# Kernel tuning notes

Measured on AMD Instinct MI355X. Metric: run time of the kernel, lower is better.

## Reference

```python
import jax, jax.numpy as jnp
import numpy as np

LEVELS = ((64, 176), (32, 88), (16, 44), (8, 22))
S_TOTAL = sum(h * w for h, w in LEVELS)  # 14960
C = 128; HH = 8; HD = 16; R = 4; L = 4; P = 8
G = 32; PC_MIN = -4.0; PC_MAX = 4.0
NUM_CLASSES = 17; PROP = 3 + 3 + 4 + 1 + NUM_CLASSES  # 28


def _ln(x, g, b):
    m = x.mean(-1, keepdims=True)
    v = ((x - m) ** 2).mean(-1, keepdims=True)
    return (x - m) * jax.lax.rsqrt(v + 1e-5) * g + b


def setup_inputs() -> dict:
    key = jax.random.key(0)
    ks = jax.random.split(key, 20)
    B, N, CAM = 1, 1024, 6
    d = {}
    d['query'] = jax.random.normal(ks[0], (B, N, C), jnp.float32)
    d['gaussian_props'] = jax.random.normal(ks[1], (B, N, PROP), jnp.float32)
    d['ms_feats'] = jax.random.normal(ks[2], (B, CAM, S_TOTAL, C), jnp.float32)
    d['depth_maps'] = jax.random.uniform(ks[3], (B, CAM, 64, 176), jnp.float32, 0.5, 50.0)
    d['lidar2img'] = jax.random.normal(ks[4], (B, CAM, 4, 4), jnp.float32)
    d['img_h'] = 256
    d['img_w'] = 704
    w = lambda k, shp: jax.random.normal(k, shp, jnp.float32) * 0.02
    d['W_sc'] = w(ks[5], (3, 3, 3, C, C)); d['b_sc'] = jnp.zeros((C,), jnp.float32)
    d['sc_g'] = jnp.ones((C,), jnp.float32); d['sc_b'] = jnp.zeros((C,), jnp.float32)
    d['ref_off_w'] = w(ks[6], (C, R * 3)); d['ref_off_b'] = jnp.zeros((R * 3,), jnp.float32)
    d['off_w'] = w(ks[7], (C, HH * R * L * P * 2)); d['off_b'] = jnp.zeros((HH * R * L * P * 2,), jnp.float32)
    d['aw_w'] = w(ks[8], (C, HH * R * L * P)); d['aw_b'] = jnp.zeros((HH * R * L * P,), jnp.float32)
    d['val_w'] = w(ks[9], (C, C)); d['val_b'] = jnp.zeros((C,), jnp.float32)
    d['out_w'] = w(ks[10], (C, C)); d['out_b'] = jnp.zeros((C,), jnp.float32)
    d['an_g'] = jnp.ones((C,), jnp.float32); d['an_b'] = jnp.zeros((C,), jnp.float32)
    d['f1_w'] = w(ks[11], (C, 4 * C)); d['f1_b'] = jnp.zeros((4 * C,), jnp.float32)
    d['f2_w'] = w(ks[12], (4 * C, C)); d['f2_b'] = jnp.zeros((C,), jnp.float32)
    d['fn_g'] = jnp.ones((C,), jnp.float32); d['fn_b'] = jnp.zeros((C,), jnp.float32)
    d['p1_w'] = w(ks[13], (C, C)); d['p1_b'] = jnp.zeros((C,), jnp.float32)
    d['p2_w'] = w(ks[14], (C, PROP)); d['p2_b'] = jnp.zeros((PROP,), jnp.float32)
    return d


def _forward(query, gaussian_props, ms_feats, depth_maps, lidar2img,
             W_sc, b_sc, sc_g, sc_b, ref_off_w, ref_off_b, off_w, off_b,
             aw_w, aw_b, val_w, val_b, out_w, out_b, an_g, an_b,
             f1_w, f1_b, f2_w, f2_b, fn_g, fn_b, p1_w, p1_b, p2_w, p2_b,
             img_h, img_w):
    B, N, _ = query.shape
    CAM = ms_feats.shape[1]
    means = gaussian_props[..., :3]
    # ---- SparseConv3DBlock: scatter-mean voxelization, 3x3x3 conv, gather back ----
    vs = (PC_MAX - PC_MIN) / G
    vox = jnp.clip(jnp.floor((means - PC_MIN) / vs).astype(jnp.int32), 0, G - 1)
    flat = (vox[..., 0] * G + vox[..., 1]) * G + vox[..., 2]  # [B,N]
    bi = jnp.arange(B)[:, None]
    grid = jnp.zeros((B, G * G * G, C), query.dtype).at[bi, flat].add(query)
    cnt = jnp.zeros((B, G * G * G, 1), query.dtype).at[bi, flat].add(1.0)
    grid = (grid / jnp.maximum(cnt, 1.0)).reshape(B, G, G, G, C)
    grid = jax.lax.conv_general_dilated(grid, W_sc, (1, 1, 1), 'SAME',
                                        dimension_numbers=('NDHWC', 'DHWIO', 'NDHWC')) + b_sc
    grid = jax.nn.gelu(grid).reshape(B, G * G * G, C)
    query = _ln(query + grid[bi, flat], sc_g, sc_b)
    # ---- DeformableAttention3D ----
    fW = jnp.asarray(img_w, query.dtype); fH = jnp.asarray(img_h, query.dtype)
    ref3d = means[:, :, None, :] + (query @ ref_off_w + ref_off_b).reshape(B, N, R, 3)
    pts = jnp.concatenate([ref3d, jnp.ones_like(ref3d[..., :1])], -1)
    proj = jnp.einsum('bcij,bnrj->bcnri', lidar2img, pts)  # [B,CAM,N,R,4]
    z = proj[..., 2]; zc = jnp.maximum(z, 1e-5)
    u = proj[..., 0] / zc; v = proj[..., 1] / zc
    valid = (z > 1e-5) & (u >= 0) & (u < fW) & (v >= 0) & (v < fH)
    Hd, Wd = depth_maps.shape[2], depth_maps.shape[3]
    iu = jnp.clip((u / fW * Wd).astype(jnp.int32), 0, Wd - 1)
    iv = jnp.clip((v / fH * Hd).astype(jnp.int32), 0, Hd - 1)
    ds = jnp.take_along_axis(depth_maps.reshape(B, CAM, Hd * Wd),
                             (iv * Wd + iu).reshape(B, CAM, N * R), axis=2).reshape(B, CAM, N, R)
    wmask = jnp.exp(-jnp.abs(z - ds)) * valid.astype(query.dtype)  # [B,CAM,N,R]
    ref2 = jnp.stack([u / fW, v / fH], -1)  # [B,CAM,N,R,2]
    offs = (query @ off_w + off_b).reshape(B, N, HH, R, L, P, 2)
    attn = jax.nn.softmax((query @ aw_w + aw_b).reshape(B, N, HH, R * L * P), -1)
    attn = attn.reshape(B, N, HH, R, L, P)
    value = (ms_feats @ val_w + val_b).reshape(B, CAM, S_TOTAL, HH, HD)
    out = jnp.zeros((B, N, HH, HD), query.dtype)
    s0 = 0
    for l, (Hl, Wl) in enumerate(LEVELS):
        sz = Hl * Wl
        vl = value[:, :, s0:s0 + sz].transpose(0, 1, 3, 2, 4).reshape(B * CAM, HH, sz, HD)
        s0 += sz
        off_l = offs[:, :, :, :, l]  # [B,N,HH,R,P,2]
        loc = ref2[:, :, :, None, :, None, :] + off_l[:, None] / jnp.array([Wl, Hl], query.dtype)
        # loc: [B,CAM,N,HH,R,P,2] in normalized coords
        x = (loc[..., 0] * Wl - 0.5).transpose(0, 1, 3, 2, 4, 5).reshape(B * CAM, HH, N * R * P)
        y = (loc[..., 1] * Hl - 0.5).transpose(0, 1, 3, 2, 4, 5).reshape(B * CAM, HH, N * R * P)
        x0 = jnp.floor(x); y0 = jnp.floor(y); wx = x - x0; wy = y - y0
        x0i = jnp.clip(x0.astype(jnp.int32), 0, Wl - 1)
        x1i = jnp.clip(x0.astype(jnp.int32) + 1, 0, Wl - 1)
        y0i = jnp.clip(y0.astype(jnp.int32), 0, Hl - 1)
        y1i = jnp.clip(y0.astype(jnp.int32) + 1, 0, Hl - 1)
        g = lambda ix, iy: jnp.take_along_axis(vl, (iy * Wl + ix)[..., None], axis=2)
        samp = (((1 - wx) * (1 - wy))[..., None] * g(x0i, y0i)
                + (wx * (1 - wy))[..., None] * g(x1i, y0i)
                + ((1 - wx) * wy)[..., None] * g(x0i, y1i)
                + (wx * wy)[..., None] * g(x1i, y1i))  # [B*CAM,HH,N*R*P,HD]
        samp = samp.reshape(B, CAM, HH, N, R, P, HD)
        ws = attn[:, :, :, :, l, :][:, None].transpose(0, 1, 3, 2, 4, 5) * wmask[:, :, None, :, :, None]
        out = out + jnp.einsum('bchnrp,bchnrpd->bnhd', ws, samp)
    attn_out = out.reshape(B, N, C) @ out_w + out_b
    query = _ln(query + attn_out, an_g, an_b)
    query = _ln(query + (jax.nn.gelu(query @ f1_w + f1_b) @ f2_w + f2_b), fn_g, fn_b)
    props = gaussian_props + (jax.nn.gelu(query @ p1_w + p1_b) @ p2_w + p2_b)
    return query, props


def reference(query, gaussian_props, ms_feats, depth_maps, lidar2img,
              W_sc, b_sc, sc_g, sc_b, ref_off_w, ref_off_b, off_w, off_b,
              aw_w, aw_b, val_w, val_b, out_w, out_b, an_g, an_b,
              f1_w, f1_b, f2_w, f2_b, fn_g, fn_b, p1_w, p1_b, p2_w, p2_b,
              img_h, img_w):
    return _forward(query, gaussian_props, ms_feats, depth_maps, lidar2img,
                    W_sc, b_sc, sc_g, sc_b, ref_off_w, ref_off_b, off_w, off_b,
                    aw_w, aw_b, val_w, val_b, out_w, out_b, an_g, an_b,
                    f1_w, f1_b, f2_w, f2_b, fn_g, fn_b, p1_w, p1_b, p2_w, p2_b,
                    img_h, img_w)
```

## Files before the change

kernel.cpp:

```cpp
#include <hip/hip_runtime.h>
#include <hip/hip_bf16.h>
#include <math.h>

#define NQ    1024
#define CC    128
#define CAM   6
#define RR    4
#define LL    4
#define PP    8
#define HHD   8
#define HDD   16
#define GG    32
#define S_TOT 14960
#define PROPN 28
#define NTAP  27

typedef __attribute__((ext_vector_type(8))) short bf16x8;
typedef __attribute__((ext_vector_type(4))) float f32x4;

__device__ __forceinline__ float gelu_tanh(float x) {
    return 0.5f * x * (1.0f + tanhf(0.7978845608028654f * (x + 0.044715f * x * x * x)));
}

__device__ __forceinline__ unsigned short f2bf(float f) {
    union { float f; unsigned int u; } x; x.f = f;
    unsigned int r = (x.u + 0x7FFFu + ((x.u >> 16) & 1u)) >> 16;
    return (unsigned short)r;
}

__device__ __forceinline__ float bf2f(short s) {
    union { unsigned int u; float f; } x;
    x.u = ((unsigned int)(unsigned short)s) << 16;
    return x.f;
}

__global__ void k_wt_scatter(const float* __restrict__ Wsc, unsigned short* __restrict__ WscT,
                             const float* __restrict__ valw, unsigned short* __restrict__ valwT,
                             const float* __restrict__ outw, unsigned short* __restrict__ outwT,
                             const float* __restrict__ p1w, unsigned short* __restrict__ p1wT,
                             const float* __restrict__ f1w, unsigned short* __restrict__ f1wT,
                             const float* __restrict__ f2w, unsigned short* __restrict__ f2wT,
                             const float* __restrict__ offw, unsigned short* __restrict__ offwT,
                             const float* __restrict__ aww, unsigned short* __restrict__ awwT,
                             const float* __restrict__ p2w, unsigned short* __restrict__ p2wT,
                             const float* __restrict__ p2b, float* __restrict__ p2bp,
                             const float* __restrict__ qin, const float* __restrict__ gp,
                             float* __restrict__ grid, float* __restrict__ cnt,
                             int* __restrict__ flatidx) {
    __shared__ float t[64][65];
    __shared__ int sflat[2];
    int z = blockIdx.z;
    int tid = threadIdx.x;

    if (z >= 63) {
        int half = tid >> 7, c = tid & 127;
        int n = ((z - 63) * 4 + (blockIdx.x * 2 + blockIdx.y)) * 2 + half;
        if (c == 0) {
            float mx = gp[n * PROPN + 0], my = gp[n * PROPN + 1], mz = gp[n * PROPN + 2];
            int vx = (int)floorf((mx + 4.0f) * 4.0f);
            int vy = (int)floorf((my + 4.0f) * 4.0f);
            int vz = (int)floorf((mz + 4.0f) * 4.0f);
            vx = min(max(vx, 0), GG - 1);
            vy = min(max(vy, 0), GG - 1);
            vz = min(max(vz, 0), GG - 1);
            int f = (vx * GG + vy) * GG + vz;
            sflat[half] = f;
            flatidx[n] = f;
            atomicAdd(&cnt[f], 1.0f);
        }
        __syncthreads();
        atomicAdd(&grid[(size_t)sflat[half] * CC + c], qin[(size_t)n * CC + c]);
        return;
    }

    int n0 = blockIdx.x * 64, k0 = blockIdx.y * 64;
    if (z == 62) {
#pragma unroll
        for (int it = 0; it < 16; ++it) {
            int idx = tid + it * 256;
            int r = idx >> 6, c = idx & 63;
            t[r][c] = (n0 + c < PROPN) ? p2w[(size_t)(k0 + r) * PROPN + n0 + c] : 0.f;
        }
        __syncthreads();
#pragma unroll
        for (int it = 0; it < 16; ++it) {
            int idx = tid + it * 256;
            int r = idx >> 6, c = idx & 63;
            p2wT[(size_t)(n0 + r) * 128 + k0 + c] = f2bf(t[c][r]);
        }
        if (blockIdx.x == 0 && blockIdx.y == 0 && tid < 128)
            p2bp[tid] = (tid < PROPN) ? p2b[tid] : 0.f;
        return;
    }
    const float* src; unsigned short* dst; int ss, ds;
    if (z < 27)       { src = Wsc + (size_t)z * 16384; dst = WscT + (size_t)z * 16384; ss = 128; ds = 128; }
    else if (z == 27) { src = valw; dst = valwT; ss = 128; ds = 128; }
    else if (z == 28) { src = outw; dst = outwT; ss = 128; ds = 128; }
    else if (z == 29) { src = p1w;  dst = p1wT;  ss = 128; ds = 128; }
    else if (z < 34)  { int q = z - 30; src = f1w + q * 128; dst = f1wT + (size_t)q * 16384; ss = 512;  ds = 128; }
    else if (z < 38)  { int q = z - 34; src = f2w + (size_t)q * 16384; dst = f2wT + q * 128; ss = 128;  ds = 512; }
    else if (z < 54)  { int q = z - 38; src = offw + q * 128; dst = offwT + (size_t)q * 16384; ss = 2048; ds = 128; }
    else              { int q = z - 54; src = aww + q * 128;  dst = awwT + (size_t)q * 16384; ss = 1024; ds = 128; }
#pragma unroll
    for (int it = 0; it < 16; ++it) {
        int idx = tid + it * 256;
        int r = idx >> 6, c = idx & 63;
        t[r][c] = src[(size_t)(k0 + r) * ss + n0 + c];
    }
    __syncthreads();
#pragma unroll
    for (int it = 0; it < 16; ++it) {
        int idx = tid + it * 256;
        int r = idx >> 6, c = idx & 63;
        dst[(size_t)(n0 + r) * ds + k0 + c] = f2bf(t[c][r]);
    }
}

__global__ __launch_bounds__(256) void k_conv1m(
    const float* __restrict__ grid, const float* __restrict__ cnt,
    const int* __restrict__ flatidx, const unsigned short* __restrict__ WT,
    float* __restrict__ convacc27) {
    __shared__ bf16x8 As[128 * 16];
    __shared__ bf16x8 Bs[128 * 16];
    __shared__ int   nbase[128];
    __shared__ float nscale[128];
    int tid = threadIdx.x;
    int tap = blockIdx.y;
    int q0 = blockIdx.x * 128;
    int dz = tap / 9 - 1, dy = (tap / 3) % 3 - 1, dx = tap % 3 - 1;

    if (tid < 128) {
        int f = flatidx[q0 + tid];
        int nx = (f >> 10) + dz, ny = ((f >> 5) & 31) + dy, nz = (f & 31) + dx;
        bool ok = (nx >= 0 && nx < GG && ny >= 0 && ny < GG && nz >= 0 && nz < GG);
        int nf = ok ? (nx * GG + ny) * GG + nz : 0;
        nbase[tid] = nf;
        nscale[tid] = ok ? 1.0f / fmaxf(cnt[nf], 1.0f) : 0.f;
    }
    __syncthreads();
#pragma unroll
    for (int it = 0; it < 8; ++it) {
        int idx = tid + it * 256;
        int m = idx >> 4, c = idx & 15;
        const float* p = grid + (size_t)nbase[m] * CC + c * 8;
        float s = nscale[m];
        float4 a = *(const float4*)p;
        float4 b = *(const float4*)(p + 4);
        bf16x8 u;
        u[0] = (short)f2bf(a.x * s); u[1] = (short)f2bf(a.y * s);
        u[2] = (short)f2bf(a.z * s); u[3] = (short)f2bf(a.w * s);
        u[4] = (short)f2bf(b.x * s); u[5] = (short)f2bf(b.y * s);
        u[6] = (short)f2bf(b.z * s); u[7] = (short)f2bf(b.w * s);
        As[m * 16 + (c ^ (m & 15))] = u;
    }
    const unsigned short* Wt = WT + (size_t)tap * CC * CC;
#pragma unroll
    for (int it = 0; it < 8; ++it) {
        int idx = tid + it * 256;
        int n = idx >> 4, c = idx & 15;
        bf16x8 w = *(const bf16x8*)(Wt + (size_t)n * CC + c * 8);
        Bs[n * 16 + (c ^ (n & 15))] = w;
    }
    __syncthreads();

    int lane = tid & 63, wv = tid >> 6;
    int wr = (wv >> 1) * 64, wc = (wv & 1) * 64;
    int r = lane & 15, q = lane >> 4;
    f32x4 acc[4][4];
#pragma unroll
    for (int i = 0; i < 4; ++i)
#pragma unroll
        for (int j = 0; j < 4; ++j)
#pragma unroll
            for (int e = 0; e < 4; ++e) acc[i][j][e] = 0.f;
#pragma unroll
    for (int ks = 0; ks < 4; ++ks) {
        bf16x8 bfr[4];
#pragma unroll
        for (int j = 0; j < 4; ++j)
            bfr[j] = Bs[(wc + j * 16 + r) * 16 + ((ks * 4 + q) ^ r)];
#pragma unroll
        for (int i = 0; i < 4; ++i) {
            bf16x8 af = As[(wr + i * 16 + r) * 16 + ((ks * 4 + q) ^ r)];
#pragma unroll
            for (int j = 0; j < 4; ++j)
                acc[i][j] = __builtin_amdgcn_mfma_f32_16x16x32_bf16(af, bfr[j], acc[i][j], 0, 0, 0);
        }
    }
    float* dst = convacc27 + (size_t)tap * NQ * CC;
#pragma unroll
    for (int i = 0; i < 4; ++i)
#pragma unroll
        for (int e = 0; e < 4; ++e) {
            int m = q0 + wr + i * 16 + q * 4 + e;
#pragma unroll
            for (int j = 0; j < 4; ++j) {
                int col = wc + j * 16 + r;
                dst[(size_t)m * CC + col] = acc[i][j][e];
            }
        }
}

__global__ void k_ln_conv_proj(const float* __restrict__ a, const float* __restrict__ convacc27,
                               const float* __restrict__ bconv,
                               const float* __restrict__ g, const float* __restrict__ be,
                               float* __restrict__ out,
                               const float* __restrict__ refw, const float* __restrict__ refb,
                               const float* __restrict__ gp, const float* __restrict__ l2i,
                               const float* __restrict__ depth,
                               const int* __restrict__ ih, const int* __restrict__ iw,
                               float* __restrict__ wm, float* __restrict__ r2u,
                               float* __restrict__ r2v) {
    int n = blockIdx.x, c = threadIdx.x;
    float apart = 0.f;
#pragma unroll
    for (int t = 0; t < NTAP; ++t) apart += convacc27[((size_t)t * NQ + n) * CC + c];
    float x = a[n * CC + c] + gelu_tanh(apart + bconv[c]);
    __shared__ float red[CC];
    __shared__ float qrow[CC];
    __shared__ float ro[12];
    red[c] = x;
    __syncthreads();
    for (int s = 64; s >= 1; s >>= 1) { if (c < s) red[c] += red[c + s]; __syncthreads(); }
    float m = red[0] * (1.0f / CC);
    __syncthreads();
    float d = x - m;
    red[c] = d * d;
    __syncthreads();
    for (int s = 64; s >= 1; s >>= 1) { if (c < s) red[c] += red[c + s]; __syncthreads(); }
    float v = red[0] * (1.0f / CC);
    float qv = d * rsqrtf(v + 1e-5f) * g[c] + be[c];
    out[n * CC + c] = qv;
    qrow[c] = qv;
    __syncthreads();
    if (c < 12) {
        float s = refb[c];
#pragma unroll 4
        for (int k = 0; k < 128; ++k) s += qrow[k] * refw[k * 12 + c];
        ro[c] = s;
    }
    __syncthreads();
    if (c < 24) {
        int cam = c >> 2, r = c & 3;
        float fH = (float)(*ih), fW = (float)(*iw);
        const float* M = l2i + cam * 16;
        float px = gp[n * PROPN + 0] + ro[r * 3 + 0];
        float py = gp[n * PROPN + 1] + ro[r * 3 + 1];
        float pz = gp[n * PROPN + 2] + ro[r * 3 + 2];
        float p0 = M[0] * px + M[1] * py + M[2]  * pz + M[3];
        float p1 = M[4] * px + M[5] * py + M[6]  * pz + M[7];
        float p2 = M[8] * px + M[9] * py + M[10] * pz + M[11];
        float zc = fmaxf(p2, 1e-5f);
        float u = p0 / zc, vv = p1 / zc;
        bool valid = (p2 > 1e-5f) && (u >= 0.f) && (u < fW) && (vv >= 0.f) && (vv < fH);
        int iu = min(max((int)(u / fW * 176.f), 0), 175);
        int iv = min(max((int)(vv / fH * 64.f), 0), 63);
        float ds = depth[cam * 64 * 176 + iv * 176 + iu];
        int o = cam * (NQ * RR) + n * RR + r;
        wm[o]  = valid ? expf(-fabsf(p2 - ds)) : 0.f;
        r2u[o] = u / fW;
        r2v[o] = vv / fH;
    }
}

__global__ __launch_bounds__(256) void k_qhead(
    const float* __restrict__ A,
    const unsigned short* __restrict__ offwT, const float* __restrict__ offb,
    unsigned short* __restrict__ offsb,
    const unsigned short* __restrict__ awwT, const float* __restrict__ awb,
    unsigned short* __restrict__ attn)
{
    __shared__ bf16x8 As[128 * 16];
    __shared__ bf16x8 Bs[128 * 16];
    __shared__ float xrow[128 * 128];
    bool isoff = blockIdx.x < 16;
    int n0 = (isoff ? blockIdx.x : (blockIdx.x - 16)) * 128;
    const unsigned short* WT = isoff ? offwT : awwT;
    int m0 = blockIdx.y * 128;
    int tid = threadIdx.x, lane = tid & 63, wv = tid >> 6;
    int wr = (wv >> 1) * 64, wc = (wv & 1) * 64;
    int r = lane & 15, q = lane >> 4;

#pragma unroll
    for (int it = 0; it < 8; ++it) {
        int idx = tid + it * 256;
        int m = idx >> 4, c = idx & 15;
        const float* p = A + (size_t)(m0 + m) * 128 + c * 8;
        float4 a = *(const float4*)p;
        float4 b = *(const float4*)(p + 4);
        bf16x8 u;
        u[0] = (short)f2bf(a.x); u[1] = (short)f2bf(a.y);
        u[2] = (short)f2bf(a.z); u[3] = (short)f2bf(a.w);
        u[4] = (short)f2bf(b.x); u[5] = (short)f2bf(b.y);
        u[6] = (short)f2bf(b.z); u[7] = (short)f2bf(b.w);
        As[m * 16 + (c ^ (m & 15))] = u;
    }
#pragma unroll
    for (int it = 0; it < 8; ++it) {
        int idx = tid + it * 256;
        int n = idx >> 4, c = idx & 15;
        Bs[n * 16 + (c ^ (n & 15))] = *(const bf16x8*)(WT + (size_t)(n0 + n) * 128 + c * 8);
    }
    __syncthreads();

    f32x4 acc[4][4];
#pragma unroll
    for (int i = 0; i < 4; ++i)
#pragma unroll
        for (int j = 0; j < 4; ++j)
#pragma unroll
            for (int e = 0; e < 4; ++e) acc[i][j][e] = 0.f;
#pragma unroll
    for (int ks = 0; ks < 4; ++ks) {
        bf16x8 bfr[4];
#pragma unroll
        for (int j = 0; j < 4; ++j)
            bfr[j] = Bs[(wc + j * 16 + r) * 16 + ((ks * 4 + q) ^ r)];
#pragma unroll
        for (int i = 0; i < 4; ++i) {
            bf16x8 af = As[(wr + i * 16 + r) * 16 + ((ks * 4 + q) ^ r)];
#pragma unroll
            for (int j = 0; j < 4; ++j)
                acc[i][j] = __builtin_amdgcn_mfma_f32_16x16x32_bf16(af, bfr[j], acc[i][j], 0, 0, 0);
        }
    }

    if (isoff) {
#pragma unroll
        for (int i = 0; i < 4; ++i)
#pragma unroll
            for (int e = 0; e < 4; ++e) {
                int m = m0 + wr + i * 16 + q * 4 + e;
#pragma unroll
                for (int j = 0; j < 4; ++j) {
                    int col = n0 + wc + j * 16 + r;
                    offsb[(size_t)m * 2048 + col] = f2bf(acc[i][j][e] + offb[col]);
                }
            }
    } else {
#pragma unroll
        for (int i = 0; i < 4; ++i)
#pragma unroll
            for (int e = 0; e < 4; ++e) {
                int ml = wr + i * 16 + q * 4 + e;
#pragma unroll
                for (int j = 0; j < 4; ++j) {
                    int cl = wc + j * 16 + r;
                    xrow[ml * 128 + cl] = acc[i][j][e] + awb[n0 + cl];
                }
            }
        __syncthreads();
        int row = tid >> 1, s = tid & 1;
        float* xr = xrow + row * 128;
        float mx = -1e30f;
#pragma unroll
        for (int e = s; e < 128; e += 2) mx = fmaxf(mx, xr[e]);
        mx = fmaxf(mx, __shfl_xor(mx, 1, 2));
        float sum = 0.f;
#pragma unroll
        for (int e = s; e < 128; e += 2) { float ee = expf(xr[e] - mx); xr[e] = ee; sum += ee; }
        sum += __shfl_xor(sum, 1, 2);
        float inv = 1.0f / sum;
        unsigned short* orow = attn + (size_t)(m0 + row) * 1024 + n0;
#pragma unroll
        for (int e = s; e < 128; e += 2) orow[e] = f2bf(xr[e] * inv);
    }
}

__global__ __launch_bounds__(256) void k_valproj(
    const float* __restrict__ A, const unsigned short* __restrict__ WT,
    const float* __restrict__ bias, unsigned short* __restrict__ out, int M)
{
    __shared__ bf16x8 Bs[128 * 16];
    __shared__ unsigned short Os[64 * 128];
    __shared__ float sbias[128];
    int tid = threadIdx.x;
    int m0 = blockIdx.x * 64;
    int lane = tid & 63, wv = tid >> 6;
    int r = lane & 15, q = lane >> 4;

#pragma unroll
    for (int it = 0; it < 8; ++it) {
        int idx = tid + it * 256;
        int n = idx >> 4, c = idx & 15;
        Bs[n * 16 + (c ^ (n & 15))] = *(const bf16x8*)(WT + (size_t)n * 128 + c * 8);
    }
    if (tid < 128) sbias[tid] = bias[tid];
    __syncthreads();

    int row = m0 + wv * 16 + r;
    int mg = min(row, M - 1);
    const float* pA = A + (size_t)mg * 128;

    f32x4 acc[8];
#pragma unroll
    for (int j = 0; j < 8; ++j)
#pragma unroll
        for (int e = 0; e < 4; ++e) acc[j][e] = 0.f;

#pragma unroll
    for (int ks = 0; ks < 4; ++ks) {
        const float* p = pA + ks * 32 + q * 8;
        float4 a = *(const float4*)p;
        float4 b = *(const float4*)(p + 4);
        bf16x8 af;
        af[0] = (short)f2bf(a.x); af[1] = (short)f2bf(a.y);
        af[2] = (short)f2bf(a.z); af[3] = (short)f2bf(a.w);
        af[4] = (short)f2bf(b.x); af[5] = (short)f2bf(b.y);
        af[6] = (short)f2bf(b.z); af[7] = (short)f2bf(b.w);
        bf16x8 bfr[8];
#pragma unroll
        for (int j = 0; j < 8; ++j)
            bfr[j] = Bs[(j * 16 + r) * 16 + ((ks * 4 + q) ^ r)];
#pragma unroll
        for (int j = 0; j < 8; ++j)
            acc[j] = __builtin_amdgcn_mfma_f32_16x16x32_bf16(af, bfr[j], acc[j], 0, 0, 0);
    }

#pragma unroll
    for (int j = 0; j < 8; ++j)
#pragma unroll
        for (int e = 0; e < 4; ++e) {
            int rl = wv * 16 + q * 4 + e;
            Os[rl * 128 + j * 16 + r] = f2bf(acc[j][e] + sbias[j * 16 + r]);
        }
    __syncthreads();
#pragma unroll
    for (int it = 0; it < 2; ++it) {
        int idx = tid + it * 256;
        int rl = idx & 63, h = idx >> 6;
        int m = m0 + rl;
        if (m < M) {
            int cam = m / S_TOT;
            int s = m - cam * S_TOT;
            int pos, HW, sb;
            if (s < 11264)      { pos = s;          HW = 11264; sb = 0; }
            else if (s < 14080) { pos = s - 11264;  HW = 2816;  sb = 11264; }
            else if (s < 14784) { pos = s - 14080;  HW = 704;   sb = 14080; }
            else                { pos = s - 14784;  HW = 176;   sb = 14784; }
            size_t dst = ((size_t)cam * S_TOT + sb) * CC
                       + (size_t)h * (HW * HDD) + (size_t)pos * HDD;
            *(bf16x8*)(out + dst)     = *(const bf16x8*)&Os[rl * 128 + h * 16];
            *(bf16x8*)(out + dst + 8) = *(const bf16x8*)&Os[rl * 128 + h * 16 + 8];
        }
    }
}

__global__ void k_sample(const unsigned short* __restrict__ value,
                         const unsigned short* __restrict__ offsb,
                         const unsigned short* __restrict__ attn,
                         const float* __restrict__ wm,
                         const float* __restrict__ r2u, const float* __restrict__ r2v,
                         float* __restrict__ sampout) {
    const int Wl_[4] = {176, 88, 44, 22};
    const int Hl_[4] = {64, 32, 16, 8};
    const int s0_[4] = {0, 11264, 14080, 14784};
    int n = blockIdx.x, tid = threadIdx.x;
    __shared__ float s_attn[1024];
    __shared__ float s_offs[2048];
    __shared__ float s_wm[24], s_ru[24], s_rv[24];

    if (tid < 128) {
        bf16x8 v = *(const bf16x8*)(attn + (size_t)n * 1024 + tid * 8);
#pragma unroll
        for (int d = 0; d < 8; ++d) s_attn[tid * 8 + d] = bf2f(v[d]);
    }
    {
        bf16x8 v = *(const bf16x8*)(offsb + (size_t)n * 2048 + tid * 8);
#pragma unroll
        for (int d = 0; d < 8; ++d) s_offs[tid * 8 + d] = bf2f(v[d]);
    }
    if (tid < 24) {
        int cam = tid >> 2, r = tid & 3;
        int o = cam * (NQ * RR) + n * RR + r;
        s_wm[tid] = wm[o]; s_ru[tid] = r2u[o]; s_rv[tid] = r2v[o];
    }
    __syncthreads();

    int h = tid >> 5, slot = tid & 31;
    int l = slot >> 3, p = slot & 7;
    int Wl = Wl_[l], Hl = Hl_[l];
    float fWl = (float)Wl, fHl = (float)Hl;
    size_t planeC = (size_t)s0_[l] * CC + (size_t)h * (Hl * Wl * HDD);
    float acc[16];
#pragma unroll
    for (int d = 0; d < 16; ++d) acc[d] = 0.f;

    for (int cr = 0; cr < 24; ++cr) {
        int cam = cr >> 2, r = cr & 3;
        float ws = s_attn[h * 128 + r * 32 + l * 8 + p] * s_wm[cr];
        if (ws == 0.f) continue;
        float ox = s_offs[h * 256 + r * 64 + l * 16 + p * 2 + 0];
        float oy = s_offs[h * 256 + r * 64 + l * 16 + p * 2 + 1];
        float x = s_ru[cr] * fWl + ox - 0.5f;
        float y = s_rv[cr] * fHl + oy - 0.5f;
        float xf = floorf(x), yf = floorf(y);
        float wx = x - xf, wy = y - yf;
        int x0 = min(max((int)xf, 0), Wl - 1);
        int x1 = min(max((int)xf + 1, 0), Wl - 1);
        int y0 = min(max((int)yf, 0), Hl - 1);
        int y1 = min(max((int)yf + 1, 0), Hl - 1);
        const unsigned short* base = value + (size_t)cam * S_TOT * CC + planeC;
        const unsigned short* p00 = base + (size_t)(y0 * Wl + x0) * HDD;
        const unsigned short* p01 = base + (size_t)(y0 * Wl + x1) * HDD;
        const unsigned short* p10 = base + (size_t)(y1 * Wl + x0) * HDD;
        const unsigned short* p11 = base + (size_t)(y1 * Wl + x1) * HDD;
        float w00 = ws * (1.f - wx) * (1.f - wy);
        float w01 = ws * wx * (1.f - wy);
        float w10 = ws * (1.f - wx) * wy;
        float w11 = ws * wx * wy;
        bf16x8 va0 = *(const bf16x8*)p00, va1 = *(const bf16x8*)(p00 + 8);
        bf16x8 vb0 = *(const bf16x8*)p01, vb1 = *(const bf16x8*)(p01 + 8);
        bf16x8 vc0 = *(const bf16x8*)p10, vc1 = *(const bf16x8*)(p10 + 8);
        bf16x8 vd0 = *(const bf16x8*)p11, vd1 = *(const bf16x8*)(p11 + 8);
#pragma unroll
        for (int d = 0; d < 8; ++d)
            acc[d] += w00 * bf2f(va0[d]) + w01 * bf2f(vb0[d]) + w10 * bf2f(vc0[d]) + w11 * bf2f(vd0[d]);
#pragma unroll
        for (int d = 0; d < 8; ++d)
            acc[8 + d] += w00 * bf2f(va1[d]) + w01 * bf2f(vb1[d]) + w10 * bf2f(vc1[d]) + w11 * bf2f(vd1[d]);
    }

#pragma unroll
    for (int d = 0; d < 16; ++d) {
        float a = acc[d];
#pragma unroll
        for (int s = 16; s >= 1; s >>= 1) a += __shfl_xor(a, s, 32);
        acc[d] = a;
    }
    if (slot == 0) {
#pragma unroll
        for (int d = 0; d < 16; ++d)
            sampout[(size_t)n * CC + h * HDD + d] = acc[d];
    }
}

__global__ __launch_bounds__(256) void k_tail(
    const float* __restrict__ sampout,
    const unsigned short* __restrict__ outwT, const float* __restrict__ outb,
    const float* __restrict__ q1, const float* __restrict__ ang, const float* __restrict__ anb,
    const unsigned short* __restrict__ f1wT, const float* __restrict__ f1b,
    const unsigned short* __restrict__ f2wT, const float* __restrict__ f2b,
    const float* __restrict__ fng, const float* __restrict__ fnb,
    const unsigned short* __restrict__ p1wT, const float* __restrict__ p1b,
    const unsigned short* __restrict__ p2wT, const float* __restrict__ p2bp,
    const float* __restrict__ gp, float* __restrict__ outq, float* __restrict__ outp)
{
    __shared__ bf16x8 As[16 * 16];
    __shared__ bf16x8 Aff[16 * 64];
    __shared__ float xrow[16 * 128];
    __shared__ float q2s[16 * 128];
    unsigned short* Affu = (unsigned short*)Aff;
    unsigned short* As2u = (unsigned short*)Aff;
    int tid = threadIdx.x, m0 = blockIdx.x * 16;
    int lane = tid & 63, wv = tid >> 6;
    int wc = wv * 32;
    int r = lane & 15, q = lane >> 4;
    int lrow = tid >> 4, ls = tid & 15;

    bf16x8 b1[2][4];
#pragma unroll
    for (int j = 0; j < 2; ++j)
#pragma unroll
        for (int ks = 0; ks < 4; ++ks)
            b1[j][ks] = *(const bf16x8*)(outwT + (size_t)(wc + j * 16 + r) * 128 + (ks * 4 + q) * 8);

    {
        int m = tid >> 4, c = tid & 15;
        const float* p = sampout + (size_t)(m0 + m) * 128 + c * 8;
        float4 a = *(const float4*)p;
        float4 b = *(const float4*)(p + 4);
        bf16x8 u;
        u[0] = (short)f2bf(a.x); u[1] = (short)f2bf(a.y);
        u[2] = (short)f2bf(a.z); u[3] = (short)f2bf(a.w);
        u[4] = (short)f2bf(b.x); u[5] = (short)f2bf(b.y);
        u[6] = (short)f2bf(b.z); u[7] = (short)f2bf(b.w);
        As[m * 16 + (c ^ m)] = u;
    }
    __syncthreads();

    f32x4 acc[2];
    bf16x8 a4[4];
#pragma unroll
    for (int ks = 0; ks < 4; ++ks) a4[ks] = As[r * 16 + ((ks * 4 + q) ^ r)];
#pragma unroll
    for (int j = 0; j < 2; ++j)
#pragma unroll
        for (int e = 0; e < 4; ++e) acc[j][e] = 0.f;
#pragma unroll
    for (int ks = 0; ks < 4; ++ks)
#pragma unroll
        for (int j = 0; j < 2; ++j)
            acc[j] = __builtin_amdgcn_mfma_f32_16x16x32_bf16(a4[ks], b1[j][ks], acc[j], 0, 0, 0);
#pragma unroll
    for (int e = 0; e < 4; ++e) {
        int ml = q * 4 + e;
#pragma unroll
        for (int j = 0; j < 2; ++j) {
            int cl = wc + j * 16 + r;
            xrow[ml * 128 + cl] = acc[j][e] + outb[cl] + q1[(size_t)(m0 + ml) * 128 + cl];
        }
    }
    __syncthreads();

    {
        float* xr = xrow + lrow * 128;
        float sum = 0.f;
#pragma unroll
        for (int e = ls; e < 128; e += 16) sum += xr[e];
#pragma unroll
        for (int d = 8; d; d >>= 1) sum += __shfl_xor(sum, d, 16);
        float mean = sum * (1.0f / 128.0f);
        float var = 0.f;
#pragma unroll
        for (int e = ls; e < 128; e += 16) { float dd = xr[e] - mean; var += dd * dd; }
#pragma unroll
        for (int d = 8; d; d >>= 1) var += __shfl_xor(var, d, 16);
        float rstd = rsqrtf(var * (1.0f / 128.0f) + 1e-5f);
#pragma unroll
        for (int e = ls; e < 128; e += 16)
            q2s[lrow * 128 + e] = (xr[e] - mean) * rstd * ang[e] + anb[e];
    }
    __syncthreads();
    {
        int m = tid >> 4, c = tid & 15;
        const float* p = q2s + m * 128 + c * 8;
        bf16x8 u;
#pragma unroll
        for (int d = 0; d < 8; ++d) u[d] = (short)f2bf(p[d]);
        As[m * 16 + (c ^ m)] = u;
    }
    __syncthreads();

#pragma unroll
    for (int ks = 0; ks < 4; ++ks) a4[ks] = As[r * 16 + ((ks * 4 + q) ^ r)];
    bf16x8 bcur[2][4];
#pragma unroll
    for (int j = 0; j < 2; ++j)
#pragma unroll
        for (int ks = 0; ks < 4; ++ks)
            bcur[j][ks] = *(const bf16x8*)(f1wT + (size_t)(wc + j * 16 + r) * 128 + (ks * 4 + q) * 8);
#pragma unroll
    for (int nt = 0; nt < 4; ++nt) {
        bf16x8 bnx[2][4];
        if (nt < 3) {
#pragma unroll
            for (int j = 0; j < 2; ++j)
#pragma unroll
                for (int ks = 0; ks < 4; ++ks)
                    bnx[j][ks] = *(const bf16x8*)(f1wT + (size_t)(nt + 1) * 16384
                                                  + (size_t)(wc + j * 16 + r) * 128 + (ks * 4 + q) * 8);
        }
#pragma unroll
        for (int j = 0; j < 2; ++j)
#pragma unroll
            for (int e = 0; e < 4; ++e) acc[j][e] = 0.f;
#pragma unroll
        for (int ks = 0; ks < 4; ++ks)
#pragma unroll
            for (int j = 0; j < 2; ++j)
                acc[j] = __builtin_amdgcn_mfma_f32_16x16x32_bf16(a4[ks], bcur[j][ks], acc[j], 0, 0, 0);
#pragma unroll
        for (int e = 0; e < 4; ++e) {
            int ml = q * 4 + e;
#pragma unroll
            for (int j = 0; j < 2; ++j) {
                int col = nt * 128 + wc + j * 16 + r;
                float v = gelu_tanh(acc[j][e] + f1b[col]);
                Affu[(ml * 64 + ((col >> 3) ^ ml)) * 8 + (col & 7)] = f2bf(v);
            }
        }
        if (nt < 3) {
#pragma unroll
            for (int j = 0; j < 2; ++j)
#pragma unroll
                for (int ks = 0; ks < 4; ++ks) bcur[j][ks] = bnx[j][ks];
        }
    }
    __syncthreads();

#pragma unroll
    for (int j = 0; j < 2; ++j)
#pragma unroll
        for (int e = 0; e < 4; ++e) acc[j][e] = 0.f;
#pragma unroll
    for (int j = 0; j < 2; ++j)
#pragma unroll
        for (int ks = 0; ks < 4; ++ks)
            bcur[j][ks] = *(const bf16x8*)(f2wT + (size_t)(wc + j * 16 + r) * 512 + (ks * 4 + q) * 8);
#pragma unroll
    for (int kc = 0; kc < 4; ++kc) {
        bf16x8 bnx[2][4];
        if (kc < 3) {
#pragma unroll
            for (int j = 0; j < 2; ++j)
#pragma unroll
                for (int ks = 0; ks < 4; ++ks)
                    bnx[j][ks] = *(const bf16x8*)(f2wT + (size_t)(wc + j * 16 + r) * 512
                                                  + ((kc + 1) * 16 + ks * 4 + q) * 8);
        }
#pragma unroll
        for (int ks = 0; ks < 4; ++ks) {
            bf16x8 af = Aff[r * 64 + ((kc * 16 + ks * 4 + q) ^ r)];
#pragma unroll
            for (int j = 0; j < 2; ++j)
                acc[j] = __builtin_amdgcn_mfma_f32_16x16x32_bf16(af, bcur[j][ks], acc[j], 0, 0, 0);
        }
        if (kc < 3) {
#pragma unroll
            for (int j = 0; j < 2; ++j)
#pragma unroll
                for (int ks = 0; ks < 4; ++ks) bcur[j][ks] = bnx[j][ks];
        }
    }
#pragma unroll
    for (int e = 0; e < 4; ++e) {
        int ml = q * 4 + e;
#pragma unroll
        for (int j = 0; j < 2; ++j) {
            int cl = wc + j * 16 + r;
            xrow[ml * 128 + cl] = acc[j][e] + f2b[cl] + q2s[ml * 128 + cl];
        }
    }
    __syncthreads();

    {
        float* xr = xrow + lrow * 128;
        float sum = 0.f;
#pragma unroll
        for (int e = ls; e < 128; e += 16) sum += xr[e];
#pragma unroll
        for (int d = 8; d; d >>= 1) sum += __shfl_xor(sum, d, 16);
        float mean = sum * (1.0f / 128.0f);
        float var = 0.f;
#pragma unroll
        for (int e = ls; e < 128; e += 16) { float dd = xr[e] - mean; var += dd * dd; }
#pragma unroll
        for (int d = 8; d; d >>= 1) var += __shfl_xor(var, d, 16);
        float rstd = rsqrtf(var * (1.0f / 128.0f) + 1e-5f);
        float* oq = outq + (size_t)(m0 + lrow) * 128;
#pragma unroll
        for (int e = ls; e < 128; e += 16) {
            float v = (xr[e] - mean) * rstd * fng[e] + fnb[e];
            oq[e] = v;
            q2s[lrow * 128 + e] = v;
        }
    }
    __syncthreads();
    {
        int m = tid >> 4, c = tid & 15;
        const float* p = q2s + m * 128 + c * 8;
        bf16x8 u;
#pragma unroll
        for (int d = 0; d < 8; ++d) u[d] = (short)f2bf(p[d]);
        As[m * 16 + (c ^ m)] = u;
    }
    __syncthreads();

#pragma unroll
    for (int ks = 0; ks < 4; ++ks) a4[ks] = As[r * 16 + ((ks * 4 + q) ^ r)];
#pragma unroll
    for (int j = 0; j < 2; ++j) {
#pragma unroll
        for (int ks = 0; ks < 4; ++ks)
            bcur[j][ks] = *(const bf16x8*)(p1wT + (size_t)(wc + j * 16 + r) * 128 + (ks * 4 + q) * 8);
#pragma unroll
        for (int e = 0; e < 4; ++e) acc[j][e] = 0.f;
    }
#pragma unroll
    for (int j = 0; j < 2; ++j)
#pragma unroll
        for (int ks = 0; ks < 4; ++ks)
            b1[j][ks] = *(const bf16x8*)(p2wT + (size_t)(wc + j * 16 + r) * 128 + (ks * 4 + q) * 8);
#pragma unroll
    for (int ks = 0; ks < 4; ++ks)
#pragma unroll
        for (int j = 0; j < 2; ++j)
            acc[j] = __builtin_amdgcn_mfma_f32_16x16x32_bf16(a4[ks], bcur[j][ks], acc[j], 0, 0, 0);
#pragma unroll
    for (int e = 0; e < 4; ++e) {
        int ml = q * 4 + e;
#pragma unroll
        for (int j = 0; j < 2; ++j) {
            int cl = wc + j * 16 + r;
            float v = gelu_tanh(acc[j][e] + p1b[cl]);
            As2u[(ml * 16 + ((cl >> 3) ^ ml)) * 8 + (cl & 7)] = f2bf(v);
        }
    }
    __syncthreads();

#pragma unroll
    for (int j = 0; j < 2; ++j)
#pragma unroll
        for (int e = 0; e < 4; ++e) acc[j][e] = 0.f;
#pragma unroll
    for (int ks = 0; ks < 4; ++ks) {
        bf16x8 af = Aff[r * 16 + ((ks * 4 + q) ^ r)];
#pragma unroll
        for (int j = 0; j < 2; ++j)
            acc[j] = __builtin_amdgcn_mfma_f32_16x16x32_bf16(af, b1[j][ks], acc[j], 0, 0, 0);
    }
#pragma unroll
    for (int e = 0; e < 4; ++e) {
        int m = m0 + q * 4 + e;
#pragma unroll
        for (int j = 0; j < 2; ++j) {
            int cl = wc + j * 16 + r;
            if (cl < PROPN)
                outp[(size_t)m * PROPN + cl] = acc[j][e] + p2bp[cl] + gp[(size_t)m * PROPN + cl];
        }
    }
}

extern "C" void kernel_launch(void* const* d_in, const int* in_sizes, int n_in,
                              void* d_out, int out_size, void* d_ws, size_t ws_size,
                              hipStream_t stream) {
    const float* query = (const float*)d_in[0];
    const float* gp    = (const float*)d_in[1];
    const float* ms    = (const float*)d_in[2];
    const float* depth = (const float*)d_in[3];
    const float* l2i   = (const float*)d_in[4];
    const int*   ih    = (const int*)d_in[5];
    const int*   iw    = (const int*)d_in[6];
    const float* Wsc   = (const float*)d_in[7];
    const float* bsc   = (const float*)d_in[8];
    const float* scg   = (const float*)d_in[9];
    const float* scb   = (const float*)d_in[10];
    const float* refw  = (const float*)d_in[11];
    const float* refb  = (const float*)d_in[12];
    const float* offw  = (const float*)d_in[13];
    const float* offbi = (const float*)d_in[14];
    const float* aww   = (const float*)d_in[15];
    const float* awb   = (const float*)d_in[16];
    const float* valw  = (const float*)d_in[17];
    const float* valb  = (const float*)d_in[18];
    const float* outw  = (const float*)d_in[19];
    const float* outb  = (const float*)d_in[20];
    const float* ang   = (const float*)d_in[21];
    const float* anb   = (const float*)d_in[22];
    const float* f1w   = (const float*)d_in[23];
    const float* f1b   = (const float*)d_in[24];
    const float* f2w   = (const float*)d_in[25];
    const float* f2b   = (const float*)d_in[26];
    const float* fng   = (const float*)d_in[27];
    const float* fnb   = (const float*)d_in[28];
    const float* p1w   = (const float*)d_in[29];
    const float* p1b   = (const float*)d_in[30];
    const float* p2w   = (const float*)d_in[31];
    const float* p2b   = (const float*)d_in[32];

    float* outq = (float*)d_out;
    float* outp = outq + NQ * CC;

    float* ws = (float*)d_ws;
    size_t o = 0;
    float* grid    = ws + o; o += (size_t)GG * GG * GG * CC;
    float* cnt     = ws + o; o += GG * GG * GG;
    size_t zero_floats = o;
    int*   flatidx = (int*)(ws + o); o += NQ;
    float* convacc27 = ws + o; o += (size_t)NTAP * NQ * CC;
    float* q1      = ws + o; o += NQ * CC;
    float* wm      = ws + o; o += CAM * NQ * RR;
    float* r2u     = ws + o; o += CAM * NQ * RR;
    float* r2v     = ws + o; o += CAM * NQ * RR;
    float* sampout = ws + o; o += NQ * CC;
    float* p2bp    = ws + o; o += 128;
    unsigned short* u16base = (unsigned short*)(ws + o);
    size_t uo = 0;
    unsigned short* value = u16base + uo; uo += (size_t)CAM * S_TOT * CC;
    unsigned short* offsb = u16base + uo; uo += (size_t)NQ * 2048;
    unsigned short* attn  = u16base + uo; uo += (size_t)NQ * 1024;
    unsigned short* offwT = u16base + uo; uo += (size_t)2048 * 128;
    unsigned short* awwT  = u16base + uo; uo += (size_t)1024 * 128;
    unsigned short* valwT = u16base + uo; uo += 128 * 128;
    unsigned short* outwT = u16base + uo; uo += 128 * 128;
    unsigned short* f1wT  = u16base + uo; uo += 512 * 128;
    unsigned short* f2wT  = u16base + uo; uo += 128 * 512;
    unsigned short* p1wT  = u16base + uo; uo += 128 * 128;
    unsigned short* p2wT  = u16base + uo; uo += 128 * 128;
    unsigned short* WscT  = u16base + uo; uo += (size_t)27 * 128 * 128;
    (void)ws_size; (void)in_sizes; (void)n_in; (void)out_size;

    hipMemsetAsync(ws, 0, zero_floats * sizeof(float), stream);

    k_wt_scatter<<<dim3(2, 2, 63 + 128), 256, 0, stream>>>(
        Wsc, WscT, valw, valwT, outw, outwT, p1w, p1wT, f1w, f1wT, f2w, f2wT,
        offw, offwT, aww, awwT, p2w, p2wT, p2b, p2bp,
        query, gp, grid, cnt, flatidx);

    k_conv1m<<<dim3(8, 27), 256, 0, stream>>>(grid, cnt, flatidx, WscT, convacc27);
    k_ln_conv_proj<<<NQ, CC, 0, stream>>>(query, convacc27, bsc, scg, scb, q1,
                                          refw, refb, gp, l2i, depth, ih, iw, wm, r2u, r2v);

    k_qhead<<<dim3(24, 8), 256, 0, stream>>>(q1, offwT, offbi, offsb, awwT, awb, attn);
    k_valproj<<<(CAM * S_TOT + 63) / 64, 256, 0, stream>>>(ms, valwT, valb, value, CAM * S_TOT);
    k_sample<<<NQ, 256, 0, stream>>>(value, offsb, attn, wm, r2u, r2v, sampout);

    k_tail<<<64, 256, 0, stream>>>(sampout, outwT, outb, q1, ang, anb,
                                   f1wT, f1b, f2wT, f2b, fng, fnb,
                                   p1wT, p1b, p2wT, p2bp, gp, outq, outp);
}
```

Before: 243.6 us.

## Use row-major value layout, register softmax in qhead, and shuffle-based layernorm

The value projection now writes rows in natural [pos][channel] order instead of a head-planar layout, and the sampler addresses with stride CC. That turns the projection epilogue into contiguous writes, but each bilinear tap in the sampler becomes a 32-byte read spread across 256-byte rows. k_qhead drops the shared A tile and the 64KB xrow buffer: each wave converts A fragments straight from global memory and does the softmax in registers with cross-lane shuffles, which lowers LDS use and may allow higher occupancy. The layernorm in k_ln_conv_proj replaces its tree reductions through shared memory with wavefront shuffle reductions, using fewer barriers.

```diff
diff --git a/kernel.cpp b/kernel.cpp
--- a/kernel.cpp
+++ b/kernel.cpp
@@ -216,28 +216,31 @@
 #pragma unroll
     for (int t = 0; t < NTAP; ++t) apart += convacc27[((size_t)t * NQ + n) * CC + c];
     float x = a[n * CC + c] + gelu_tanh(apart + bconv[c]);
-    __shared__ float red[CC];
+    __shared__ float w4[4];
     __shared__ float qrow[CC];
     __shared__ float ro[12];
-    red[c] = x;
-    __syncthreads();
-    for (int s = 64; s >= 1; s >>= 1) { if (c < s) red[c] += red[c + s]; __syncthreads(); }
-    float m = red[0] * (1.0f / CC);
-    __syncthreads();
-    float d = x - m;
-    red[c] = d * d;
-    __syncthreads();
-    for (int s = 64; s >= 1; s >>= 1) { if (c < s) red[c] += red[c + s]; __syncthreads(); }
-    float v = red[0] * (1.0f / CC);
-    float qv = d * rsqrtf(v + 1e-5f) * g[c] + be[c];
+    float s = x;
+#pragma unroll
+    for (int d = 1; d < 64; d <<= 1) s += __shfl_xor(s, d);
+    if ((c & 63) == 0) w4[c >> 6] = s;
+    __syncthreads();
+    float m = (w4[0] + w4[1]) * (1.0f / CC);
+    float dd = x - m;
+    float v = dd * dd;
+#pragma unroll
+    for (int d = 1; d < 64; d <<= 1) v += __shfl_xor(v, d);
+    if ((c & 63) == 0) w4[2 + (c >> 6)] = v;
+    __syncthreads();
+    float var = (w4[2] + w4[3]) * (1.0f / CC);
+    float qv = dd * rsqrtf(var + 1e-5f) * g[c] + be[c];
     out[n * CC + c] = qv;
     qrow[c] = qv;
     __syncthreads();
     if (c < 12) {
-        float s = refb[c];
+        float sacc = refb[c];
 #pragma unroll 4
-        for (int k = 0; k < 128; ++k) s += qrow[k] * refw[k * 12 + c];
-        ro[c] = s;
+        for (int k = 0; k < 128; ++k) sacc += qrow[k] * refw[k * 12 + c];
+        ro[c] = sacc;
     }
     __syncthreads();
     if (c < 24) {
@@ -270,31 +273,15 @@
     const unsigned short* __restrict__ awwT, const float* __restrict__ awb,
     unsigned short* __restrict__ attn)
 {
-    __shared__ bf16x8 As[128 * 16];
     __shared__ bf16x8 Bs[128 * 16];
-    __shared__ float xrow[128 * 128];
     bool isoff = blockIdx.x < 16;
     int n0 = (isoff ? blockIdx.x : (blockIdx.x - 16)) * 128;
     const unsigned short* WT = isoff ? offwT : awwT;
     int m0 = blockIdx.y * 128;
     int tid = threadIdx.x, lane = tid & 63, wv = tid >> 6;
-    int wr = (wv >> 1) * 64, wc = (wv & 1) * 64;
     int r = lane & 15, q = lane >> 4;
-
-#pragma unroll
-    for (int it = 0; it < 8; ++it) {
-        int idx = tid + it * 256;
-        int m = idx >> 4, c = idx & 15;
-        const float* p = A + (size_t)(m0 + m) * 128 + c * 8;
-        float4 a = *(const float4*)p;
-        float4 b = *(const float4*)(p + 4);
-        bf16x8 u;
-        u[0] = (short)f2bf(a.x); u[1] = (short)f2bf(a.y);
-        u[2] = (short)f2bf(a.z); u[3] = (short)f2bf(a.w);
-        u[4] = (short)f2bf(b.x); u[5] = (short)f2bf(b.y);
-        u[6] = (short)f2bf(b.z); u[7] = (short)f2bf(b.w);
-        As[m * 16 + (c ^ (m & 15))] = u;
-    }
+    int mw = m0 + wv * 32;
+
 #pragma unroll
     for (int it = 0; it < 8; ++it) {
         int idx = tid + it * 256;
@@ -303,67 +290,77 @@
     }
     __syncthreads();
 
-    f32x4 acc[4][4];
-#pragma unroll
-    for (int i = 0; i < 4; ++i)
-#pragma unroll
-        for (int j = 0; j < 4; ++j)
+    f32x4 acc[2][8];
+#pragma unroll
+    for (int i = 0; i < 2; ++i)
+#pragma unroll
+        for (int j = 0; j < 8; ++j)
 #pragma unroll
             for (int e = 0; e < 4; ++e) acc[i][j][e] = 0.f;
+
 #pragma unroll
     for (int ks = 0; ks < 4; ++ks) {
-        bf16x8 bfr[4];
-#pragma unroll
-        for (int j = 0; j < 4; ++j)
-            bfr[j] = Bs[(wc + j * 16 + r) * 16 + ((ks * 4 + q) ^ r)];
-#pragma unroll
-        for (int i = 0; i < 4; ++i) {
-            bf16x8 af = As[(wr + i * 16 + r) * 16 + ((ks * 4 + q) ^ r)];
-#pragma unroll
-            for (int j = 0; j < 4; ++j)
-                acc[i][j] = __builtin_amdgcn_mfma_f32_16x16x32_bf16(af, bfr[j], acc[i][j], 0, 0, 0);
-        }
-    }
+        bf16x8 af[2];
+#pragma unroll
+        for (int i = 0; i < 2; ++i) {
+            const float* p = A + (size_t)(mw + i * 16 + r) * 128 + (ks * 4 + q) * 8;
+            float4 a = *(const float4*)p;
+            float4 b = *(const float4*)(p + 4);
+            bf16x8 u;
+            u[0] = (short)f2bf(a.x); u[1] = (short)f2bf(a.y);
+            u[2] = (short)f2bf(a.z); u[3] = (short)f2bf(a.w);
+            u[4] = (short)f2bf(b.x); u[5] = (short)f2bf(b.y);
+            u[6] = (short)f2bf(b.z); u[7] = (short)f2bf(b.w);
+            af[i] = u;
+        }
+#pragma unroll
+        for (int j = 0; j < 8; ++j) {
+            bf16x8 b = Bs[(j * 16 + r) * 16 + ((ks * 4 + q) ^ r)];
+#pragma unroll
+            for (int i = 0; i < 2; ++i)
+                acc[i][j] = __builtin_amdgcn_mfma_f32_16x16x32_bf16(af[i], b, acc[i][j], 0, 0, 0);
+        }
+    }
+
+    float bia[8];
+    const float* bsrc = isoff ? offb : awb;
+#pragma unroll
+    for (int j = 0; j < 8; ++j) bia[j] = bsrc[n0 + j * 16 + r];
 
     if (isoff) {
 #pragma unroll
-        for (int i = 0; i < 4; ++i)
+        for (int i = 0; i < 2; ++i)
 #pragma unroll
             for (int e = 0; e < 4; ++e) {
-                int m = m0 + wr + i * 16 + q * 4 + e;
-#pragma unroll
-                for (int j = 0; j < 4; ++j) {
-                    int col = n0 + wc + j * 16 + r;
-                    offsb[(size_t)m * 2048 + col] = f2bf(acc[i][j][e] + offb[col]);
-                }
+                int m = mw + i * 16 + q * 4 + e;
+                unsigned short* orow = offsb + (size_t)m * 2048 + n0;
+#pragma unroll
+                for (int j = 0; j < 8; ++j)
+                    orow[j * 16 + r] = f2bf(acc[i][j][e] + bia[j]);
             }
     } else {
 #pragma unroll
-        for (int i = 0; i < 4; ++i)
+        for (int i = 0; i < 2; ++i)
 #pragma unroll
             for (int e = 0; e < 4; ++e) {
-                int ml = wr + i * 16 + q * 4 + e;
-#pragma unroll
-                for (int j = 0; j < 4; ++j) {
-                    int cl = wc + j * 16 + r;
-                    xrow[ml * 128 + cl] = acc[i][j][e] + awb[n0 + cl];
-                }
+                float mx = -1e30f;
+#pragma unroll
+                for (int j = 0; j < 8; ++j) mx = fmaxf(mx, acc[i][j][e] + bia[j]);
+#pragma unroll
+                for (int d = 1; d < 16; d <<= 1) mx = fmaxf(mx, __shfl_xor(mx, d));
+                float ex[8];
+                float sum = 0.f;
+#pragma unroll
+                for (int j = 0; j < 8; ++j) { ex[j] = expf(acc[i][j][e] + bia[j] - mx); sum += ex[j]; }
+#pragma unroll
+                for (int d = 1; d < 16; d <<= 1) sum += __shfl_xor(sum, d);
+                float inv = 1.0f / sum;
+                int m = mw + i * 16 + q * 4 + e;
+                unsigned short* orow = attn + (size_t)m * 1024 + n0;
+#pragma unroll
+                for (int j = 0; j < 8; ++j)
+                    orow[j * 16 + r] = f2bf(ex[j] * inv);
             }
-        __syncthreads();
-        int row = tid >> 1, s = tid & 1;
-        float* xr = xrow + row * 128;
-        float mx = -1e30f;
-#pragma unroll
-        for (int e = s; e < 128; e += 2) mx = fmaxf(mx, xr[e]);
-        mx = fmaxf(mx, __shfl_xor(mx, 1, 2));
-        float sum = 0.f;
-#pragma unroll
-        for (int e = s; e < 128; e += 2) { float ee = expf(xr[e] - mx); xr[e] = ee; sum += ee; }
-        sum += __shfl_xor(sum, 1, 2);
-        float inv = 1.0f / sum;
-        unsigned short* orow = attn + (size_t)(m0 + row) * 1024 + n0;
-#pragma unroll
-        for (int e = s; e < 128; e += 2) orow[e] = f2bf(xr[e] * inv);
     }
 }
 
@@ -426,23 +423,12 @@
         }
     __syncthreads();
 #pragma unroll
-    for (int it = 0; it < 2; ++it) {
+    for (int it = 0; it < 4; ++it) {
         int idx = tid + it * 256;
-        int rl = idx & 63, h = idx >> 6;
+        int rl = idx >> 4, ch = idx & 15;
         int m = m0 + rl;
-        if (m < M) {
-            int cam = m / S_TOT;
-            int s = m - cam * S_TOT;
-            int pos, HW, sb;
-            if (s < 11264)      { pos = s;          HW = 11264; sb = 0; }
-            else if (s < 14080) { pos = s - 11264;  HW = 2816;  sb = 11264; }
-            else if (s < 14784) { pos = s - 14080;  HW = 704;   sb = 14080; }
-            else                { pos = s - 14784;  HW = 176;   sb = 14784; }
-            size_t dst = ((size_t)cam * S_TOT + sb) * CC
-                       + (size_t)h * (HW * HDD) + (size_t)pos * HDD;
-            *(bf16x8*)(out + dst)     = *(const bf16x8*)&Os[rl * 128 + h * 16];
-            *(bf16x8*)(out + dst + 8) = *(const bf16x8*)&Os[rl * 128 + h * 16 + 8];
-        }
+        if (m < M)
+            *(bf16x8*)(out + (size_t)m * 128 + ch * 8) = *(const bf16x8*)&Os[rl * 128 + ch * 8];
     }
 }
 
@@ -481,7 +467,6 @@
     int l = slot >> 3, p = slot & 7;
     int Wl = Wl_[l], Hl = Hl_[l];
     float fWl = (float)Wl, fHl = (float)Hl;
-    size_t planeC = (size_t)s0_[l] * CC + (size_t)h * (Hl * Wl * HDD);
     float acc[16];
 #pragma unroll
     for (int d = 0; d < 16; ++d) acc[d] = 0.f;
@@ -500,11 +485,11 @@
         int x1 = min(max((int)xf + 1, 0), Wl - 1);
         int y0 = min(max((int)yf, 0), Hl - 1);
         int y1 = min(max((int)yf + 1, 0), Hl - 1);
-        const unsigned short* base = value + (size_t)cam * S_TOT * CC + planeC;
-        const unsigned short* p00 = base + (size_t)(y0 * Wl + x0) * HDD;
-        const unsigned short* p01 = base + (size_t)(y0 * Wl + x1) * HDD;
-        const unsigned short* p10 = base + (size_t)(y1 * Wl + x0) * HDD;
-        const unsigned short* p11 = base + (size_t)(y1 * Wl + x1) * HDD;
+        size_t b = ((size_t)cam * S_TOT + s0_[l]) * CC + h * HDD;
+        const unsigned short* p00 = value + b + (size_t)(y0 * Wl + x0) * CC;
+        const unsigned short* p01 = value + b + (size_t)(y0 * Wl + x1) * CC;
+        const unsigned short* p10 = value + b + (size_t)(y1 * Wl + x0) * CC;
+        const unsigned short* p11 = value + b + (size_t)(y1 * Wl + x1) * CC;
         float w00 = ws * (1.f - wx) * (1.f - wy);
         float w01 = ws * wx * (1.f - wy);
         float w10 = ws * (1.f - wx) * wy;
```

Measured after the change: 227.5 us. 6.6% less time.
